# Kernel optimization log

Hardware: AMD Instinct MI355X
Metric: run time of the kernel (lower is better)

Reference implementation:

```python
import jax, jax.numpy as jnp
import numpy as np

ALPHA, GAMMA = 0.25, 2.0
THR = 0.85            # soft_target_threshold
KL_EPS = 1e-6
FOCAL_EPS = 1e-8
VOC = 96              # len(vocab); index VOC is blank/pad


def setup_inputs() -> dict:
    key = jax.random.key(0)
    ks = jax.random.split(key, 6)
    bs, nq, n_pts, num_gt, L = 16, 200, 25, 32, 25
    return {
        "pred_logits": jax.random.normal(ks[0], (bs, nq, n_pts, 1), jnp.float32),
        "pred_ctrl_points": jax.random.uniform(ks[1], (bs, nq, n_pts, 2), jnp.float32),
        "pred_text_logits": jax.random.normal(ks[2], (bs, nq, n_pts, VOC + 1), jnp.float32),
        "tgt_ctrl_points": jax.random.uniform(ks[3], (bs, num_gt, n_pts, 2), jnp.float32),
        "tgt_texts": jax.random.randint(ks[4], (bs, num_gt, L), 0, VOC + 1),
        "centroids": jax.random.normal(ks[5], (VOC, 256), jnp.float32),
    }


def _cost_matrix(pred_logits, pred_ctrl_points, pred_text_logits,
                 tgt_ctrl_points, tgt_texts, centroids):
    bs, nq, n_pts, _ = pred_logits.shape
    num_gt = tgt_texts.shape[1]

    # ---- focal classification cost (mean over control points) ----
    out_prob = jax.nn.sigmoid(pred_logits.reshape(bs * nq, n_pts, -1))
    neg = (1.0 - ALPHA) * out_prob ** GAMMA * (-jnp.log1p(-(out_prob - FOCAL_EPS)))
    neg = (1.0 - ALPHA) * out_prob ** GAMMA * (-jnp.log(1.0 - out_prob + FOCAL_EPS))
    pos = ALPHA * (1.0 - out_prob) ** GAMMA * (-jnp.log(out_prob + FOCAL_EPS))
    cost_class = (pos[..., 0] - neg[..., 0]).mean(-1, keepdims=True)  # [bs*nq, 1]

    # ---- L1 cdist over flattened control points ----
    out_pts = pred_ctrl_points.reshape(bs * nq, n_pts * 2)
    tgt_pts = tgt_ctrl_points.reshape(bs * num_gt, n_pts * 2)
    cost_kpts = jnp.abs(out_pts[:, None, :] - tgt_pts[None, :, :]).sum(-1)  # [bs*nq, bs*num_gt]

    # ---- linguistic KL-div cost (per-batch block diagonal) ----
    probs = jax.nn.softmax(pred_text_logits, axis=-1)          # [bs,nq,n_pts,VOC+1]
    pred_avg = probs[..., :VOC].mean(axis=2)                   # [bs,nq,VOC]
    P = pred_avg + KL_EPS
    P = P / P.sum(-1, keepdims=True)
    logP = jnp.log(P)

    # soft target distribution per character (generate_soft_target_sequence)
    cn = centroids / jnp.linalg.norm(centroids, axis=-1, keepdims=True)
    soft_all = THR * jnp.eye(VOC, dtype=P.dtype) + (1.0 - THR) * jax.nn.softmax(cn @ cn.T, axis=-1)  # [VOC,VOC]

    mask = (tgt_texts != VOC)                                  # [bs,num_gt,L]
    lengths = mask.sum(-1)                                     # [bs,num_gt]
    per_char = soft_all[jnp.clip(tgt_texts, 0, VOC - 1)]       # [bs,num_gt,L,VOC]
    tgt_avg = (per_char * mask[..., None]).sum(2) / jnp.maximum(lengths, 1)[..., None].astype(P.dtype)
    T = tgt_avg + KL_EPS
    T = T / T.sum(-1, keepdims=True)                           # [bs,num_gt,VOC]

    # KL(T || P) = sum T*logT - sum T*logP, vectorized over (query, gt)
    kl = (T * jnp.log(T)).sum(-1)[:, None, :] - jnp.einsum('bqv,bgv->bqg', logP, T)  # [bs,nq,num_gt]
    kl = jnp.where(lengths[:, None, :] == 0, 100.0, kl)

    # place per-batch blocks on the diagonal of the global cost matrix
    eye = jnp.eye(bs, dtype=kl.dtype)
    cost_text = jnp.einsum('bqg,bc->bqcg', kl, eye).reshape(bs * nq, bs * num_gt)

    C = 1.0 * cost_class + 1.0 * cost_kpts + 1.0 * cost_text   # class/coord/text weights = 1
    return C.reshape(bs, nq, bs * num_gt)


def reference(pred_logits, pred_ctrl_points, pred_text_logits,
              tgt_ctrl_points, tgt_texts, centroids):
    return _cost_matrix(pred_logits, pred_ctrl_points, pred_text_logits,
                        tgt_ctrl_points, tgt_texts, centroids)
```

## Files before the change

kernel.cpp:

```cpp
#include <hip/hip_runtime.h>
#include <hip/hip_bf16.h>

#define BS 16
#define NQ 200
#define NPTS 25
#define VOC 96
#define VOCP1 97
#define NGT 32
#define LSEQ 25
#define NCOL (BS*NGT)
#define NBQ (BS*NQ)
#define KL_EPS 1e-6f
#define FOCAL_EPS 1e-8f

__global__ __launch_bounds__(128) void k1_pred(
        const float* __restrict__ pred_logits,
        const float* __restrict__ pred_text_logits,
        float* __restrict__ logP,
        float* __restrict__ cost_class)
{
    const int bq  = blockIdx.x;
    const int tid = threadIdx.x;
    __shared__ float s_exp[NPTS * VOCP1];
    __shared__ float s_invden[NPTS];
    __shared__ float s_red[128];

    const float* tl = pred_text_logits + (size_t)bq * NPTS * VOCP1;
    for (int i = tid; i < NPTS * VOCP1; i += 128)
        s_exp[i] = __expf(tl[i]);
    __syncthreads();

    if (tid < NPTS) {
        float s = 0.f;
        const float* row = s_exp + tid * VOCP1;
        for (int v = 0; v < VOCP1; v++) s += row[v];
        s_invden[tid] = 1.0f / s;
    }

    float cc = 0.f;
    if (tid < NPTS) {
        float x = pred_logits[bq * NPTS + tid];
        float p = 1.f / (1.f + __expf(-x));
        float pos = 0.25f * (1.f - p) * (1.f - p) * (-__logf(p + FOCAL_EPS));
        float neg = 0.75f * p * p * (-__logf(1.f - p + FOCAL_EPS));
        cc = pos - neg;
    }
    s_red[tid] = cc;
    __syncthreads();
    for (int s = 64; s > 0; s >>= 1) {
        if (tid < s) s_red[tid] += s_red[tid + s];
        __syncthreads();
    }
    if (tid == 0) cost_class[bq] = s_red[0] * (1.0f / NPTS);

    float avg = 0.f;
    if (tid < VOC) {
        float a = 0.f;
        for (int p = 0; p < NPTS; p++)
            a += s_exp[p * VOCP1 + tid] * s_invden[p];
        avg = a * (1.0f / NPTS);
    }
    __syncthreads();
    s_red[tid] = avg;
    __syncthreads();
    for (int s = 64; s > 0; s >>= 1) {
        if (tid < s) s_red[tid] += s_red[tid + s];
        __syncthreads();
    }
    float denom = s_red[0] + (float)VOC * KL_EPS;
    if (tid < VOC)
        logP[(size_t)bq * VOC + tid] = __logf((avg + KL_EPS) / denom);
}

__global__ __launch_bounds__(128) void k2a_soft(
        const float* __restrict__ centroids,
        float* __restrict__ soft)
{
    const int i   = blockIdx.x;
    const int tid = threadIdx.x;
    __shared__ float row[256];
    __shared__ float s_red[128];
    for (int k = tid; k < 256; k += 128) row[k] = centroids[i * 256 + k];
    __syncthreads();

    float e = 0.f;
    if (tid < VOC) {
        float dij = 0.f, djj = 0.f, dii = 0.f;
        const float* cj = centroids + tid * 256;
        for (int k = 0; k < 256; k++) {
            float a = row[k], b = cj[k];
            dij += a * b; djj += b * b; dii += a * a;
        }
        float sim = dij * rsqrtf(dii * djj);
        e = __expf(sim);
    }
    s_red[tid] = e;
    __syncthreads();
    for (int s = 64; s > 0; s >>= 1) {
        if (tid < s) s_red[tid] += s_red[tid + s];
        __syncthreads();
    }
    if (tid < VOC) {
        float v = 0.15f * e / s_red[0];
        if (tid == i) v += 0.85f;
        soft[i * VOC + tid] = v;
    }
}

__global__ __launch_bounds__(128) void k2b_T(
        const int* __restrict__ tgt_texts,
        const float* __restrict__ soft,
        float* __restrict__ T,
        float* __restrict__ TlogT,
        int* __restrict__ lens)
{
    const int bg  = blockIdx.x;
    const int tid = threadIdx.x;
    __shared__ float s_red[128];
    __shared__ int   s_chars[LSEQ];
    __shared__ int   s_len;

    if (tid < LSEQ) s_chars[tid] = tgt_texts[bg * LSEQ + tid];
    __syncthreads();
    if (tid == 0) {
        int c = 0;
        for (int l = 0; l < LSEQ; l++) if (s_chars[l] != VOC) c++;
        s_len = c;
    }
    __syncthreads();

    float avg = 0.f;
    if (tid < VOC) {
        float a = 0.f;
        for (int l = 0; l < LSEQ; l++) {
            int t = s_chars[l];
            if (t != VOC) a += soft[t * VOC + tid];
        }
        int len = s_len;
        avg = a / (float)(len > 0 ? len : 1);
    }
    s_red[tid] = avg;
    __syncthreads();
    for (int s = 64; s > 0; s >>= 1) {
        if (tid < s) s_red[tid] += s_red[tid + s];
        __syncthreads();
    }
    float denom = s_red[0] + (float)VOC * KL_EPS;
    float tl = 0.f;
    if (tid < VOC) {
        float t = (avg + KL_EPS) / denom;
        T[(size_t)bg * VOC + tid] = t;
        tl = t * __logf(t);
    }
    __syncthreads();
    s_red[tid] = tl;
    __syncthreads();
    for (int s = 64; s > 0; s >>= 1) {
        if (tid < s) s_red[tid] += s_red[tid + s];
        __syncthreads();
    }
    if (tid == 0) {
        TlogT[bg] = s_red[0];
        lens[bg]  = s_len;
    }
}

__global__ __launch_bounds__(256) void k3_cost(
        const float* __restrict__ pred_ctrl,
        const float* __restrict__ tgt_ctrl,
        const float* __restrict__ logP,
        const float* __restrict__ cost_class,
        const float* __restrict__ T,
        const float* __restrict__ TlogT,
        const int* __restrict__ lens,
        float* __restrict__ out)
{
    const int bq  = blockIdx.x;
    const int b   = bq / NQ;
    const int tid = threadIdx.x;
    __shared__ float s_pts[50];
    __shared__ float s_logP[VOC];

    if (tid < 50) s_pts[tid] = pred_ctrl[bq * 50 + tid];
    if (tid >= 64 && tid < 64 + VOC) s_logP[tid - 64] = logP[(size_t)bq * VOC + (tid - 64)];
    __syncthreads();

    const float cc = cost_class[bq];

    for (int j = tid; j < NCOL; j += 256) {
        const int cb = j >> 5;
        const float* tp = tgt_ctrl + j * 50;
        float kp = 0.f;
        for (int d = 0; d < 50; d++) kp += fabsf(s_pts[d] - tp[d]);
        float text = 0.f;
        if (cb == b) {
            if (lens[j] == 0) {
                text = 100.f;
            } else {
                const float* Trow = T + (size_t)j * VOC;
                float dot = 0.f;
                for (int v = 0; v < VOC; v++) dot += s_logP[v] * Trow[v];
                text = TlogT[j] - dot;
            }
        }
        out[(size_t)bq * NCOL + j] = cc + kp + text;
    }
}

extern "C" void kernel_launch(void* const* d_in, const int* in_sizes, int n_in,
                              void* d_out, int out_size, void* d_ws, size_t ws_size,
                              hipStream_t stream) {
    const float* pred_logits = (const float*)d_in[0];
    const float* pred_ctrl   = (const float*)d_in[1];
    const float* pred_text   = (const float*)d_in[2];
    const float* tgt_ctrl    = (const float*)d_in[3];
    const int*   tgt_texts   = (const int*)d_in[4];
    const float* centroids   = (const float*)d_in[5];
    float* out = (float*)d_out;

    float* ws        = (float*)d_ws;
    float* logP      = ws;
    float* costclass = logP + (size_t)NBQ * VOC;
    float* soft      = costclass + NBQ;
    float* T         = soft + VOC * VOC;
    float* TlogT     = T + (size_t)NCOL * VOC;
    int*   lens      = (int*)(TlogT + NCOL);

    k1_pred<<<NBQ, 128, 0, stream>>>(pred_logits, pred_text, logP, costclass);
    k2a_soft<<<VOC, 128, 0, stream>>>(centroids, soft);
    k2b_T<<<NCOL, 128, 0, stream>>>(tgt_texts, soft, T, TlogT, lens);
    k3_cost<<<NBQ, 256, 0, stream>>>(pred_ctrl, tgt_ctrl, logP, costclass,
                                     T, TlogT, lens, out);
}
```

Measured before the change: 139.3 us.

## Tile cost kernel over row blocks and use wave-shuffle reductions

The cost kernel now gives each block 25 query rows and 256 target columns. Each thread holds one target's 50 coordinates in registers and reuses them across all rows, and the text KL dot products for the block are staged through shared memory. This replaces the old one-row-per-block layout, where every block re-read the full target control-point array from memory. The helper kernels also switch their tree reductions in shared memory to wave shuffles and use vectorized centroid loads. In exchange, k3 runs far fewer blocks (256) and uses heavy register and shared-memory footprints, which may limit occupancy.

```diff
diff --git a/kernel.cpp b/kernel.cpp
--- a/kernel.cpp
+++ b/kernel.cpp
@@ -19,55 +19,58 @@
         float* __restrict__ logP,
         float* __restrict__ cost_class)
 {
-    const int bq  = blockIdx.x;
-    const int tid = threadIdx.x;
+    const int bq   = blockIdx.x;
+    const int tid  = threadIdx.x;
+    const int wave = tid >> 6, lane = tid & 63;
     __shared__ float s_exp[NPTS * VOCP1];
     __shared__ float s_invden[NPTS];
-    __shared__ float s_red[128];
+    __shared__ float s_part[2];
 
     const float* tl = pred_text_logits + (size_t)bq * NPTS * VOCP1;
     for (int i = tid; i < NPTS * VOCP1; i += 128)
         s_exp[i] = __expf(tl[i]);
     __syncthreads();
 
-    if (tid < NPTS) {
+    const int grp = tid >> 5, sub = tid & 31;
+    for (int p0 = 0; p0 < NPTS; p0 += 4) {
+        int p = p0 + grp;
         float s = 0.f;
-        const float* row = s_exp + tid * VOCP1;
-        for (int v = 0; v < VOCP1; v++) s += row[v];
-        s_invden[tid] = 1.0f / s;
-    }
-
-    float cc = 0.f;
-    if (tid < NPTS) {
-        float x = pred_logits[bq * NPTS + tid];
-        float p = 1.f / (1.f + __expf(-x));
-        float pos = 0.25f * (1.f - p) * (1.f - p) * (-__logf(p + FOCAL_EPS));
-        float neg = 0.75f * p * p * (-__logf(1.f - p + FOCAL_EPS));
-        cc = pos - neg;
-    }
-    s_red[tid] = cc;
-    __syncthreads();
-    for (int s = 64; s > 0; s >>= 1) {
-        if (tid < s) s_red[tid] += s_red[tid + s];
-        __syncthreads();
-    }
-    if (tid == 0) cost_class[bq] = s_red[0] * (1.0f / NPTS);
+        if (p < NPTS)
+            for (int v = sub; v < VOCP1; v += 32) s += s_exp[p * VOCP1 + v];
+        #pragma unroll
+        for (int off = 16; off; off >>= 1) s += __shfl_xor(s, off);
+        if (p < NPTS && sub == 0) s_invden[p] = 1.0f / s;
+    }
+
+    if (wave == 0) {
+        float cc = 0.f;
+        if (lane < NPTS) {
+            float x = pred_logits[bq * NPTS + lane];
+            float p = 1.f / (1.f + __expf(-x));
+            float pos = 0.25f * (1.f - p) * (1.f - p) * (-__logf(p + FOCAL_EPS));
+            float neg = 0.75f * p * p * (-__logf(1.f - p + FOCAL_EPS));
+            cc = pos - neg;
+        }
+        #pragma unroll
+        for (int off = 32; off; off >>= 1) cc += __shfl_xor(cc, off);
+        if (lane == 0) cost_class[bq] = cc * (1.0f / NPTS);
+    }
+    __syncthreads();
 
     float avg = 0.f;
     if (tid < VOC) {
         float a = 0.f;
+        #pragma unroll
         for (int p = 0; p < NPTS; p++)
             a += s_exp[p * VOCP1 + tid] * s_invden[p];
         avg = a * (1.0f / NPTS);
     }
-    __syncthreads();
-    s_red[tid] = avg;
-    __syncthreads();
-    for (int s = 64; s > 0; s >>= 1) {
-        if (tid < s) s_red[tid] += s_red[tid + s];
-        __syncthreads();
-    }
-    float denom = s_red[0] + (float)VOC * KL_EPS;
+    float s = avg;
+    #pragma unroll
+    for (int off = 32; off; off >>= 1) s += __shfl_xor(s, off);
+    if (lane == 0) s_part[wave] = s;
+    __syncthreads();
+    float denom = s_part[0] + s_part[1] + (float)VOC * KL_EPS;
     if (tid < VOC)
         logP[(size_t)bq * VOC + tid] = __logf((avg + KL_EPS) / denom);
 }
@@ -78,30 +81,36 @@
 {
     const int i   = blockIdx.x;
     const int tid = threadIdx.x;
+    const int wave = tid >> 6, lane = tid & 63;
     __shared__ float row[256];
-    __shared__ float s_red[128];
-    for (int k = tid; k < 256; k += 128) row[k] = centroids[i * 256 + k];
+    __shared__ float s_part[2];
+    for (int k = tid; k < 64; k += 128)
+        *(float4*)&row[k * 4] = *(const float4*)&centroids[i * 256 + k * 4];
     __syncthreads();
 
     float e = 0.f;
     if (tid < VOC) {
         float dij = 0.f, djj = 0.f, dii = 0.f;
-        const float* cj = centroids + tid * 256;
-        for (int k = 0; k < 256; k++) {
-            float a = row[k], b = cj[k];
-            dij += a * b; djj += b * b; dii += a * a;
+        const float4* cj = (const float4*)(centroids + (size_t)tid * 256);
+        #pragma unroll 4
+        for (int k = 0; k < 64; k++) {
+            float4 b = cj[k];
+            float4 a = *(const float4*)&row[k * 4];
+            dij += a.x * b.x + a.y * b.y + a.z * b.z + a.w * b.w;
+            djj += b.x * b.x + b.y * b.y + b.z * b.z + b.w * b.w;
+            dii += a.x * a.x + a.y * a.y + a.z * a.z + a.w * a.w;
         }
         float sim = dij * rsqrtf(dii * djj);
         e = __expf(sim);
     }
-    s_red[tid] = e;
-    __syncthreads();
-    for (int s = 64; s > 0; s >>= 1) {
-        if (tid < s) s_red[tid] += s_red[tid + s];
-        __syncthreads();
-    }
-    if (tid < VOC) {
-        float v = 0.15f * e / s_red[0];
+    float s = e;
+    #pragma unroll
+    for (int off = 32; off; off >>= 1) s += __shfl_xor(s, off);
+    if (lane == 0) s_part[wave] = s;
+    __syncthreads();
+    float den = s_part[0] + s_part[1];
+    if (tid < VOC) {
+        float v = 0.15f * e / den;
         if (tid == i) v += 0.85f;
         soft[i * VOC + tid] = v;
     }
@@ -114,20 +123,22 @@
         float* __restrict__ TlogT,
         int* __restrict__ lens)
 {
-    const int bg  = blockIdx.x;
-    const int tid = threadIdx.x;
-    __shared__ float s_red[128];
+    const int bg   = blockIdx.x;
+    const int tid  = threadIdx.x;
+    const int wave = tid >> 6, lane = tid & 63;
+    __shared__ float s_part[2];
     __shared__ int   s_chars[LSEQ];
     __shared__ int   s_len;
 
     if (tid < LSEQ) s_chars[tid] = tgt_texts[bg * LSEQ + tid];
     __syncthreads();
-    if (tid == 0) {
-        int c = 0;
-        for (int l = 0; l < LSEQ; l++) if (s_chars[l] != VOC) c++;
-        s_len = c;
-    }
-    __syncthreads();
+    if (wave == 0) {
+        int t = (lane < LSEQ) ? s_chars[lane] : VOC;
+        unsigned long long m = __ballot(t != VOC);
+        if (lane == 0) s_len = __popcll(m);
+    }
+    __syncthreads();
+    const int len = s_len;
 
     float avg = 0.f;
     if (tid < VOC) {
@@ -136,35 +147,34 @@
             int t = s_chars[l];
             if (t != VOC) a += soft[t * VOC + tid];
         }
-        int len = s_len;
         avg = a / (float)(len > 0 ? len : 1);
     }
-    s_red[tid] = avg;
-    __syncthreads();
-    for (int s = 64; s > 0; s >>= 1) {
-        if (tid < s) s_red[tid] += s_red[tid + s];
-        __syncthreads();
-    }
-    float denom = s_red[0] + (float)VOC * KL_EPS;
+    float s = avg;
+    #pragma unroll
+    for (int off = 32; off; off >>= 1) s += __shfl_xor(s, off);
+    if (lane == 0) s_part[wave] = s;
+    __syncthreads();
+    float denom = s_part[0] + s_part[1] + (float)VOC * KL_EPS;
+    float t = (avg + KL_EPS) / denom;
     float tl = 0.f;
     if (tid < VOC) {
-        float t = (avg + KL_EPS) / denom;
         T[(size_t)bg * VOC + tid] = t;
         tl = t * __logf(t);
     }
     __syncthreads();
-    s_red[tid] = tl;
-    __syncthreads();
-    for (int s = 64; s > 0; s >>= 1) {
-        if (tid < s) s_red[tid] += s_red[tid + s];
-        __syncthreads();
-    }
+    float s2 = tl;
+    #pragma unroll
+    for (int off = 32; off; off >>= 1) s2 += __shfl_xor(s2, off);
+    if (lane == 0) s_part[wave] = s2;
+    __syncthreads();
     if (tid == 0) {
-        TlogT[bg] = s_red[0];
-        lens[bg]  = s_len;
-    }
-}
-
+        TlogT[bg] = s_part[0] + s_part[1];
+        lens[bg]  = len;
+    }
+}
+
+#define K3_ROWS 25
+#define K3_COLS 256
 __global__ __launch_bounds__(256) void k3_cost(
         const float* __restrict__ pred_ctrl,
         const float* __restrict__ tgt_ctrl,
@@ -175,35 +185,90 @@
         const int* __restrict__ lens,
         float* __restrict__ out)
 {
-    const int bq  = blockIdx.x;
-    const int b   = bq / NQ;
-    const int tid = threadIdx.x;
-    __shared__ float s_pts[50];
-    __shared__ float s_logP[VOC];
-
-    if (tid < 50) s_pts[tid] = pred_ctrl[bq * 50 + tid];
-    if (tid >= 64 && tid < 64 + VOC) s_logP[tid - 64] = logP[(size_t)bq * VOC + (tid - 64)];
-    __syncthreads();
-
-    const float cc = cost_class[bq];
-
-    for (int j = tid; j < NCOL; j += 256) {
-        const int cb = j >> 5;
-        const float* tp = tgt_ctrl + j * 50;
-        float kp = 0.f;
-        for (int d = 0; d < 50; d++) kp += fabsf(s_pts[d] - tp[d]);
-        float text = 0.f;
-        if (cb == b) {
-            if (lens[j] == 0) {
-                text = 100.f;
+    const int rt   = blockIdx.x >> 1;
+    const int ch   = blockIdx.x & 1;
+    const int row0 = rt * K3_ROWS;
+    const int c0   = ch * K3_COLS;
+    const int b    = rt >> 3;
+    const int tid  = threadIdx.x;
+    const int col  = c0 + tid;
+
+    __shared__ float s_pred[K3_ROWS][52];
+    __shared__ float s_logP[K3_ROWS][VOC];
+    __shared__ float s_T[NGT][VOCP1];
+    __shared__ float s_text[K3_ROWS][33];
+    __shared__ float s_cc[K3_ROWS];
+
+    const bool has_text = ((b < 8) == (ch == 0));
+    const int  jb0 = b * NGT - c0;
+
+    const float* pg = pred_ctrl + (size_t)row0 * 50;
+    for (int i = tid; i < K3_ROWS * 50; i += 256) {
+        int r = i / 50, d = i - r * 50;
+        s_pred[r][d] = pg[i];
+    }
+    if (tid < K3_ROWS) s_cc[tid] = cost_class[row0 + tid];
+    if (has_text) {
+        for (int i = tid; i < K3_ROWS * VOC; i += 256) {
+            int r = i / VOC, v = i - r * VOC;
+            s_logP[r][v] = logP[(size_t)(row0 + r) * VOC + v];
+        }
+        for (int i = tid; i < NGT * VOC; i += 256) {
+            int g = i / VOC, v = i - g * VOC;
+            s_T[g][v] = T[(size_t)(b * NGT + g) * VOC + v];
+        }
+    }
+
+    float tg[50];
+    {
+        const float2* trow = (const float2*)(tgt_ctrl + (size_t)col * 50);
+        #pragma unroll
+        for (int q = 0; q < 25; q++) {
+            float2 v = trow[q];
+            tg[2 * q] = v.x; tg[2 * q + 1] = v.y;
+        }
+    }
+    __syncthreads();
+
+    if (has_text) {
+        for (int i = tid; i < K3_ROWS * NGT; i += 256) {
+            int r = i >> 5, g = i & 31;
+            int c = b * NGT + g;
+            float txt;
+            if (lens[c] == 0) {
+                txt = 100.f;
             } else {
-                const float* Trow = T + (size_t)j * VOC;
-                float dot = 0.f;
-                for (int v = 0; v < VOC; v++) dot += s_logP[v] * Trow[v];
-                text = TlogT[j] - dot;
+                float d0 = 0.f, d1 = 0.f;
+                #pragma unroll
+                for (int v = 0; v < VOC; v += 2) {
+                    d0 += s_logP[r][v]     * s_T[g][v];
+                    d1 += s_logP[r][v + 1] * s_T[g][v + 1];
+                }
+                txt = TlogT[c] - (d0 + d1);
             }
-        }
-        out[(size_t)bq * NCOL + j] = cc + kp + text;
+            s_text[r][g] = txt;
+        }
+        __syncthreads();
+    }
+
+    for (int r = 0; r < K3_ROWS; r++) {
+        float kp0 = 0.f, kp1 = 0.f, kp2 = 0.f, kp3 = 0.f;
+        #pragma unroll
+        for (int q = 0; q < 12; q++) {
+            float4 p = *(const float4*)&s_pred[r][q * 4];
+            kp0 += fabsf(p.x - tg[q * 4 + 0]);
+            kp1 += fabsf(p.y - tg[q * 4 + 1]);
+            kp2 += fabsf(p.z - tg[q * 4 + 2]);
+            kp3 += fabsf(p.w - tg[q * 4 + 3]);
+        }
+        kp0 += fabsf(s_pred[r][48] - tg[48]);
+        kp1 += fabsf(s_pred[r][49] - tg[49]);
+        float val = s_cc[r] + (kp0 + kp1) + (kp2 + kp3);
+        if (has_text) {
+            unsigned g = (unsigned)(tid - jb0);
+            if (g < (unsigned)NGT) val += s_text[r][g];
+        }
+        out[(size_t)(row0 + r) * NCOL + col] = val;
     }
 }
 
@@ -229,6 +294,6 @@
     k1_pred<<<NBQ, 128, 0, stream>>>(pred_logits, pred_text, logP, costclass);
     k2a_soft<<<VOC, 128, 0, stream>>>(centroids, soft);
     k2b_T<<<NCOL, 128, 0, stream>>>(tgt_texts, soft, T, TlogT, lens);
-    k3_cost<<<NBQ, 256, 0, stream>>>(pred_ctrl, tgt_ctrl, logP, costclass,
+    k3_cost<<<256, 256, 0, stream>>>(pred_ctrl, tgt_ctrl, logP, costclass,
                                      T, TlogT, lens, out);
 }
```

Result: faster. 132.0 us (-5.3%).
